# Kernel tuning notes

Measured on AMD Instinct MI355X. Metric: run time of the kernel, lower is better.

## Reference

```python
import jax, jax.numpy as jnp
import numpy as np

B, CAP, D, A, K = 512, 50000, 256, 18, 5
LAM = 0.5  # ration_lambda


def setup_inputs() -> dict:
    key = jax.random.key(0)
    ks = jax.random.split(key, 14)
    def w(k, shape, fan_in):
        return jax.random.normal(k, shape, dtype=jnp.float32) / np.sqrt(fan_in)
    inp = {
        'x': jax.random.normal(ks[0], (B, 4, 84, 84), dtype=jnp.float32),
        'conv1_w': w(ks[1], (32, 4, 8, 8), 4 * 8 * 8),
        'conv1_b': jnp.zeros((32,), jnp.float32),
        'conv2_w': w(ks[2], (64, 32, 4, 4), 32 * 4 * 4),
        'conv2_b': jnp.zeros((64,), jnp.float32),
        'conv3_w': w(ks[3], (64, 64, 3, 3), 64 * 3 * 3),
        'conv3_b': jnp.zeros((64,), jnp.float32),
        'fc_w': w(ks[4], (3136, D), 3136),
        'fc_b': jnp.zeros((D,), jnp.float32),
        'out_w': w(ks[5], (D, A), D),
        'out_b': jnp.zeros((A,), jnp.float32),
        # value buffer: stored embeddings (post-ReLU, nonnegative) and Q values
        'buf_emb': jax.random.uniform(ks[6], (CAP, D), dtype=jnp.float32),
        'buf_q': jax.random.normal(ks[7], (CAP, A), dtype=jnp.float32),
    }
    return inp


def _conv_relu(x, w, b, stride):
    y = jax.lax.conv_general_dilated(
        x, w, window_strides=(stride, stride), padding='VALID',
        dimension_numbers=('NCHW', 'OIHW', 'NCHW'))
    return jax.nn.relu(y + b[None, :, None, None])


def reference(x, conv1_w, conv1_b, conv2_w, conv2_b, conv3_w, conv3_b,
              fc_w, fc_b, out_w, out_b, buf_emb, buf_q):
    # LargeAtariCNN: 84->20->9->7 spatial, ReLU everywhere incl. final linear
    h = _conv_relu(x, conv1_w, conv1_b, 4)   # [B,32,20,20]
    h = _conv_relu(h, conv2_w, conv2_b, 2)   # [B,64,9,9]
    h = _conv_relu(h, conv3_w, conv3_b, 1)   # [B,64,7,7]
    h = h.reshape(h.shape[0], -1)            # [B,3136]
    h = jax.nn.relu(h @ fc_w + fc_b)         # [B,D] embedding
    q = h @ out_w + out_b                    # [B,A] parametric Q
    # kNN over value buffer: squared L2 distances [B,CAP]
    d2 = (jnp.sum(h * h, axis=1, keepdims=True)
          - 2.0 * (h @ buf_emb.T)
          + jnp.sum(buf_emb * buf_emb, axis=1)[None, :])
    _, idx = jax.lax.top_k(-d2, K)           # K nearest, [B,K]
    non_param_q = jnp.mean(buf_q[idx], axis=1)  # [B,K,A] -> [B,A]
    q_blend = LAM * q + (1.0 - LAM) * non_param_q
    return (q_blend, h)
```

## Files before the change

### kernel.cpp

```cpp
#include <hip/hip_runtime.h>
#include <hip/hip_bf16.h>

#define FINF 3.402823466e38f

typedef short bf16x8 __attribute__((ext_vector_type(8)));
typedef float f32x4 __attribute__((ext_vector_type(4)));

__device__ __forceinline__ unsigned short f2bf_rne(float f) {
  unsigned u = __float_as_uint(f);
  unsigned r = u + 0x7fff + ((u >> 16) & 1);
  return (unsigned short)(r >> 16);
}
__device__ __forceinline__ float bf2f(unsigned short u) {
  return __uint_as_float(((unsigned)u) << 16);
}
__device__ __forceinline__ unsigned long long shflx64(unsigned long long v, int m) {
  unsigned lo = __shfl_xor((unsigned)(v & 0xFFFFFFFFu), m, 64);
  unsigned hi = __shfl_xor((unsigned)(v >> 32), m, 64);
  return (((unsigned long long)hi) << 32) | lo;
}
__device__ __forceinline__ void lds_barrier() {
  asm volatile("s_waitcnt lgkmcnt(0)" ::: "memory");
  __builtin_amdgcn_s_barrier();
  __builtin_amdgcn_sched_barrier(0);
}
__device__ __forceinline__ void wave_sync() {
  asm volatile("s_waitcnt lgkmcnt(0)" ::: "memory");
  __builtin_amdgcn_sched_barrier(0);
}
__device__ __forceinline__ void gload16(const unsigned short* g, short* l) {
  __builtin_amdgcn_global_load_lds(
      (const __attribute__((address_space(1))) unsigned int*)g,
      (__attribute__((address_space(3))) unsigned int*)l, 16, 0, 0);
}

__global__ __launch_bounds__(128) void w1swz_k(const float* __restrict__ w1,
                                               unsigned short* __restrict__ bh,
                                               unsigned short* __restrict__ bl) {
  int ky = blockIdx.x;
  int t = threadIdx.x, nf = t >> 6, l = t & 63;
  int oc = nf * 16 + (l & 15), ic = l >> 4;
  bf16x8 hv, lv;
#pragma unroll
  for (int j = 0; j < 8; ++j) {
    float v = w1[((oc * 4 + ic) * 8 + ky) * 8 + j];
    unsigned short h = f2bf_rne(v);
    hv[j] = (short)h;
    lv[j] = (short)f2bf_rne(v - bf2f(h));
  }
  *(bf16x8*)(&bh[((size_t)(ky * 2 + nf) * 64 + l) * 8]) = hv;
  *(bf16x8*)(&bl[((size_t)(ky * 2 + nf) * 64 + l) * 8]) = lv;
}

__global__ __launch_bounds__(256) void conv1m_k(
    const float* __restrict__ x,
    const unsigned short* __restrict__ bh, const unsigned short* __restrict__ bl,
    const float* __restrict__ bias, unsigned short* __restrict__ h1s) {
  __shared__ short As[256 * 72];
  int t = threadIdx.x, w = t >> 6, lane = t & 63, lm = lane & 15, hi4 = lane >> 4;
  int m = blockIdx.x * 256 + t;
  int n = m / 400, p = m % 400, oy = p / 20, ox = p % 20;
  size_t xoff = (size_t)n * 28224 + (size_t)(oy * 4) * 84 + ox * 4;
  f32x4 acc[4][2];
#pragma unroll
  for (int mf = 0; mf < 4; ++mf)
#pragma unroll
    for (int nf = 0; nf < 2; ++nf) acc[mf][nf] = (f32x4){0.f, 0.f, 0.f, 0.f};

  float4 fa[8];
#pragma unroll
  for (int ic = 0; ic < 4; ++ic) {
    fa[ic * 2 + 0] = *(const float4*)(x + xoff + ic * 7056);
    fa[ic * 2 + 1] = *(const float4*)(x + xoff + ic * 7056 + 4);
  }
  const unsigned short* bfp = bh + (size_t)lane * 8;
  const unsigned short* blp = bl + (size_t)lane * 8;
  bf16x8 cbh[2], cbl[2];
#pragma unroll
  for (int nf = 0; nf < 2; ++nf) {
    cbh[nf] = *(const bf16x8*)(bfp + nf * 512);
    cbl[nf] = *(const bf16x8*)(blp + nf * 512);
  }
#pragma unroll
  for (int ky = 0; ky < 8; ++ky) {
    if (ky) wave_sync();
    {
      short* wp = &As[t * 72];
#pragma unroll
      for (int ic = 0; ic < 4; ++ic) {
        float e0 = fa[ic * 2].x, e1 = fa[ic * 2].y, e2 = fa[ic * 2].z, e3 = fa[ic * 2].w;
        float e4 = fa[ic * 2 + 1].x, e5 = fa[ic * 2 + 1].y, e6 = fa[ic * 2 + 1].z, e7 = fa[ic * 2 + 1].w;
        bf16x8 hv, lv;
        unsigned short h;
        h = f2bf_rne(e0); hv[0] = (short)h; lv[0] = (short)f2bf_rne(e0 - bf2f(h));
        h = f2bf_rne(e1); hv[1] = (short)h; lv[1] = (short)f2bf_rne(e1 - bf2f(h));
        h = f2bf_rne(e2); hv[2] = (short)h; lv[2] = (short)f2bf_rne(e2 - bf2f(h));
        h = f2bf_rne(e3); hv[3] = (short)h; lv[3] = (short)f2bf_rne(e3 - bf2f(h));
        h = f2bf_rne(e4); hv[4] = (short)h; lv[4] = (short)f2bf_rne(e4 - bf2f(h));
        h = f2bf_rne(e5); hv[5] = (short)h; lv[5] = (short)f2bf_rne(e5 - bf2f(h));
        h = f2bf_rne(e6); hv[6] = (short)h; lv[6] = (short)f2bf_rne(e6 - bf2f(h));
        h = f2bf_rne(e7); hv[7] = (short)h; lv[7] = (short)f2bf_rne(e7 - bf2f(h));
        *(bf16x8*)(wp + ic * 8) = hv;
        *(bf16x8*)(wp + 36 + ic * 8) = lv;
      }
    }
    wave_sync();
    bf16x8 nbh[2], nbl[2];
    if (ky < 7) {
      size_t ap = xoff + (size_t)(ky + 1) * 84;
#pragma unroll
      for (int ic = 0; ic < 4; ++ic) {
        fa[ic * 2 + 0] = *(const float4*)(x + ap + ic * 7056);
        fa[ic * 2 + 1] = *(const float4*)(x + ap + ic * 7056 + 4);
      }
#pragma unroll
      for (int nf = 0; nf < 2; ++nf) {
        nbh[nf] = *(const bf16x8*)(bfp + ((ky + 1) * 2 + nf) * 512);
        nbl[nf] = *(const bf16x8*)(blp + ((ky + 1) * 2 + nf) * 512);
      }
    }
    bf16x8 ah[4], al[4];
#pragma unroll
    for (int mf = 0; mf < 4; ++mf) {
      const short* rp = &As[(w * 64 + mf * 16 + lm) * 72 + hi4 * 8];
      ah[mf] = *(const bf16x8*)(rp);
      al[mf] = *(const bf16x8*)(rp + 36);
    }
#pragma unroll
    for (int mf = 0; mf < 4; ++mf)
#pragma unroll
      for (int nf = 0; nf < 2; ++nf) {
        acc[mf][nf] = __builtin_amdgcn_mfma_f32_16x16x32_bf16(ah[mf], cbh[nf], acc[mf][nf], 0, 0, 0);
        acc[mf][nf] = __builtin_amdgcn_mfma_f32_16x16x32_bf16(ah[mf], cbl[nf], acc[mf][nf], 0, 0, 0);
        acc[mf][nf] = __builtin_amdgcn_mfma_f32_16x16x32_bf16(al[mf], cbh[nf], acc[mf][nf], 0, 0, 0);
      }
    if (ky < 7) {
#pragma unroll
      for (int nf = 0; nf < 2; ++nf) { cbh[nf] = nbh[nf]; cbl[nf] = nbl[nf]; }
    }
  }
  float bv[2];
#pragma unroll
  for (int nf = 0; nf < 2; ++nf) bv[nf] = bias[nf * 16 + lm];
#pragma unroll
  for (int mf = 0; mf < 4; ++mf)
#pragma unroll
    for (int nf = 0; nf < 2; ++nf)
#pragma unroll
      for (int r = 0; r < 4; ++r) {
        size_t mrow = (size_t)blockIdx.x * 256 + w * 64 + mf * 16 + hi4 * 4 + r;
        float v = fmaxf(acc[mf][nf][r] + bv[nf], 0.f);
        unsigned short h = f2bf_rne(v);
        h1s[mrow * 64 + nf * 16 + lm] = h;
        h1s[mrow * 64 + 32 + nf * 16 + lm] = f2bf_rne(v - bf2f(h));
      }
}

__global__ __launch_bounds__(256) void w2swz_k(const float* __restrict__ w2,
                                               unsigned short* __restrict__ bh,
                                               unsigned short* __restrict__ bl) {
  int tap = blockIdx.x, ky = tap >> 2, kx = tap & 3;
  int t = threadIdx.x, nf = t >> 6, l = t & 63;
  int oc = nf * 16 + (l & 15);
  bf16x8 hv, lv;
#pragma unroll
  for (int j = 0; j < 8; ++j) {
    int ic = (l >> 4) * 8 + j;
    float v = w2[((oc * 32 + ic) * 4 + ky) * 4 + kx];
    unsigned short h = f2bf_rne(v);
    hv[j] = (short)h;
    lv[j] = (short)f2bf_rne(v - bf2f(h));
  }
  *(bf16x8*)(&bh[((size_t)(tap * 4 + nf) * 64 + l) * 8]) = hv;
  *(bf16x8*)(&bl[((size_t)(tap * 4 + nf) * 64 + l) * 8]) = lv;
}

__global__ __launch_bounds__(256) void w3swz_k(const float* __restrict__ w3,
                                               unsigned short* __restrict__ bh,
                                               unsigned short* __restrict__ bl) {
  int tt = blockIdx.x, tap = tt >> 1, half = tt & 1, ky = tap / 3, kx = tap % 3;
  int t = threadIdx.x, nf = t >> 6, l = t & 63;
  int oc = nf * 16 + (l & 15);
  bf16x8 hv, lv;
#pragma unroll
  for (int j = 0; j < 8; ++j) {
    int ic = half * 32 + (l >> 4) * 8 + j;
    float v = w3[((oc * 64 + ic) * 3 + ky) * 3 + kx];
    unsigned short h = f2bf_rne(v);
    hv[j] = (short)h;
    lv[j] = (short)f2bf_rne(v - bf2f(h));
  }
  *(bf16x8*)(&bh[((size_t)(tt * 4 + nf) * 64 + l) * 8]) = hv;
  *(bf16x8*)(&bl[((size_t)(tt * 4 + nf) * 64 + l) * 8]) = lv;
}

__global__ __launch_bounds__(256) void conv2m_k(
    const unsigned short* __restrict__ h1s, const unsigned short* __restrict__ bh,
    const unsigned short* __restrict__ bl, const float* __restrict__ bias,
    unsigned short* __restrict__ h2s) {
  __shared__ short As[256 * 72];
  int t = threadIdx.x, w = t >> 6, lane = t & 63, lm = lane & 15, hi4 = lane >> 4;
  int m = blockIdx.x * 256 + t;
  int n = m / 81, p = m % 81, oy = p / 9, ox = p % 9;
  const unsigned short* abase = h1s + (size_t)(n * 400 + oy * 40 + ox * 2) * 64;
  f32x4 acc[4][4];
#pragma unroll
  for (int mf = 0; mf < 4; ++mf)
#pragma unroll
    for (int nf = 0; nf < 4; ++nf) acc[mf][nf] = (f32x4){0.f, 0.f, 0.f, 0.f};

  bf16x8 s0, s1, s2, s3, s4, s5, s6, s7;
  {
    const unsigned short* ap = abase;
    s0 = *(const bf16x8*)(ap);      s1 = *(const bf16x8*)(ap + 8);
    s2 = *(const bf16x8*)(ap + 16); s3 = *(const bf16x8*)(ap + 24);
    s4 = *(const bf16x8*)(ap + 32); s5 = *(const bf16x8*)(ap + 40);
    s6 = *(const bf16x8*)(ap + 48); s7 = *(const bf16x8*)(ap + 56);
  }
  const unsigned short* bfp = bh + (size_t)lane * 8;
  const unsigned short* blp = bl + (size_t)lane * 8;
  bf16x8 cbh[4], cbl[4];
#pragma unroll
  for (int nf = 0; nf < 4; ++nf) {
    cbh[nf] = *(const bf16x8*)(bfp + nf * 512);
    cbl[nf] = *(const bf16x8*)(blp + nf * 512);
  }
#pragma unroll
  for (int tap = 0; tap < 16; ++tap) {
    if (tap) wave_sync();
    {
      short* wp = &As[t * 72];
      *(bf16x8*)(wp) = s0;      *(bf16x8*)(wp + 8) = s1;
      *(bf16x8*)(wp + 16) = s2; *(bf16x8*)(wp + 24) = s3;
      *(bf16x8*)(wp + 36) = s4; *(bf16x8*)(wp + 44) = s5;
      *(bf16x8*)(wp + 52) = s6; *(bf16x8*)(wp + 60) = s7;
    }
    wave_sync();
    bf16x8 nbh[4], nbl[4];
    if (tap < 15) {
      const unsigned short* ap = abase + (((tap + 1) >> 2) * 1280 + ((tap + 1) & 3) * 64);
      s0 = *(const bf16x8*)(ap);      s1 = *(const bf16x8*)(ap + 8);
      s2 = *(const bf16x8*)(ap + 16); s3 = *(const bf16x8*)(ap + 24);
      s4 = *(const bf16x8*)(ap + 32); s5 = *(const bf16x8*)(ap + 40);
      s6 = *(const bf16x8*)(ap + 48); s7 = *(const bf16x8*)(ap + 56);
#pragma unroll
      for (int nf = 0; nf < 4; ++nf) {
        nbh[nf] = *(const bf16x8*)(bfp + ((tap + 1) * 4 + nf) * 512);
        nbl[nf] = *(const bf16x8*)(blp + ((tap + 1) * 4 + nf) * 512);
      }
    }
    bf16x8 ah[4], al[4];
#pragma unroll
    for (int mf = 0; mf < 4; ++mf) {
      const short* rp = &As[(w * 64 + mf * 16 + lm) * 72 + hi4 * 8];
      ah[mf] = *(const bf16x8*)(rp);
      al[mf] = *(const bf16x8*)(rp + 36);
    }
#pragma unroll
    for (int mf = 0; mf < 4; ++mf)
#pragma unroll
      for (int nf = 0; nf < 4; ++nf) {
        acc[mf][nf] = __builtin_amdgcn_mfma_f32_16x16x32_bf16(ah[mf], cbh[nf], acc[mf][nf], 0, 0, 0);
        acc[mf][nf] = __builtin_amdgcn_mfma_f32_16x16x32_bf16(ah[mf], cbl[nf], acc[mf][nf], 0, 0, 0);
        acc[mf][nf] = __builtin_amdgcn_mfma_f32_16x16x32_bf16(al[mf], cbh[nf], acc[mf][nf], 0, 0, 0);
      }
    if (tap < 15) {
#pragma unroll
      for (int nf = 0; nf < 4; ++nf) { cbh[nf] = nbh[nf]; cbl[nf] = nbl[nf]; }
    }
  }
  float bv[4];
#pragma unroll
  for (int nf = 0; nf < 4; ++nf) bv[nf] = bias[nf * 16 + lm];
#pragma unroll
  for (int mf = 0; mf < 4; ++mf)
#pragma unroll
    for (int nf = 0; nf < 4; ++nf)
#pragma unroll
      for (int r = 0; r < 4; ++r) {
        size_t mrow = (size_t)blockIdx.x * 256 + w * 64 + mf * 16 + hi4 * 4 + r;
        float v = fmaxf(acc[mf][nf][r] + bv[nf], 0.f);
        unsigned short h = f2bf_rne(v);
        h2s[mrow * 128 + nf * 16 + lm] = h;
        h2s[mrow * 128 + 64 + nf * 16 + lm] = f2bf_rne(v - bf2f(h));
      }
}

__global__ __launch_bounds__(256) void conv3m_k(
    const unsigned short* __restrict__ h2s, const unsigned short* __restrict__ bh,
    const unsigned short* __restrict__ bl, const float* __restrict__ bias,
    unsigned short* __restrict__ h3hi, unsigned short* __restrict__ h3lo) {
  __shared__ short As[256 * 72];
  int t = threadIdx.x, w = t >> 6, lane = t & 63, lm = lane & 15, hi4 = lane >> 4;
  int m = blockIdx.x * 256 + t;
  int n = m / 49, p = m % 49, oy = p / 7, ox = p % 7;
  const unsigned short* abase = h2s + (size_t)(n * 81 + oy * 9 + ox) * 128;
  f32x4 acc[4][4];
#pragma unroll
  for (int mf = 0; mf < 4; ++mf)
#pragma unroll
    for (int nf = 0; nf < 4; ++nf) acc[mf][nf] = (f32x4){0.f, 0.f, 0.f, 0.f};

  bf16x8 s0, s1, s2, s3, s4, s5, s6, s7;
  {
    const unsigned short* ap = abase;
    s0 = *(const bf16x8*)(ap);      s1 = *(const bf16x8*)(ap + 8);
    s2 = *(const bf16x8*)(ap + 16); s3 = *(const bf16x8*)(ap + 24);
    s4 = *(const bf16x8*)(ap + 64); s5 = *(const bf16x8*)(ap + 72);
    s6 = *(const bf16x8*)(ap + 80); s7 = *(const bf16x8*)(ap + 88);
  }
  const unsigned short* bfp = bh + (size_t)lane * 8;
  const unsigned short* blp = bl + (size_t)lane * 8;
  bf16x8 cbh[4], cbl[4];
#pragma unroll
  for (int nf = 0; nf < 4; ++nf) {
    cbh[nf] = *(const bf16x8*)(bfp + nf * 512);
    cbl[nf] = *(const bf16x8*)(blp + nf * 512);
  }
#pragma unroll
  for (int tt = 0; tt < 18; ++tt) {
    if (tt) wave_sync();
    {
      short* wp = &As[t * 72];
      *(bf16x8*)(wp) = s0;      *(bf16x8*)(wp + 8) = s1;
      *(bf16x8*)(wp + 16) = s2; *(bf16x8*)(wp + 24) = s3;
      *(bf16x8*)(wp + 36) = s4; *(bf16x8*)(wp + 44) = s5;
      *(bf16x8*)(wp + 52) = s6; *(bf16x8*)(wp + 60) = s7;
    }
    wave_sync();
    bf16x8 nbh[4], nbl[4];
    if (tt < 17) {
      const int tn = tt + 1, tapn = tn >> 1, halfn = tn & 1;
      const unsigned short* ap = abase + ((tapn / 3) * 9 + (tapn % 3)) * 128 + halfn * 32;
      s0 = *(const bf16x8*)(ap);      s1 = *(const bf16x8*)(ap + 8);
      s2 = *(const bf16x8*)(ap + 16); s3 = *(const bf16x8*)(ap + 24);
      s4 = *(const bf16x8*)(ap + 64); s5 = *(const bf16x8*)(ap + 72);
      s6 = *(const bf16x8*)(ap + 80); s7 = *(const bf16x8*)(ap + 88);
#pragma unroll
      for (int nf = 0; nf < 4; ++nf) {
        nbh[nf] = *(const bf16x8*)(bfp + ((tt + 1) * 4 + nf) * 512);
        nbl[nf] = *(const bf16x8*)(blp + ((tt + 1) * 4 + nf) * 512);
      }
    }
    bf16x8 ah[4], al[4];
#pragma unroll
    for (int mf = 0; mf < 4; ++mf) {
      const short* rp = &As[(w * 64 + mf * 16 + lm) * 72 + hi4 * 8];
      ah[mf] = *(const bf16x8*)(rp);
      al[mf] = *(const bf16x8*)(rp + 36);
    }
#pragma unroll
    for (int mf = 0; mf < 4; ++mf)
#pragma unroll
      for (int nf = 0; nf < 4; ++nf) {
        acc[mf][nf] = __builtin_amdgcn_mfma_f32_16x16x32_bf16(ah[mf], cbh[nf], acc[mf][nf], 0, 0, 0);
        acc[mf][nf] = __builtin_amdgcn_mfma_f32_16x16x32_bf16(ah[mf], cbl[nf], acc[mf][nf], 0, 0, 0);
        acc[mf][nf] = __builtin_amdgcn_mfma_f32_16x16x32_bf16(al[mf], cbh[nf], acc[mf][nf], 0, 0, 0);
      }
    if (tt < 17) {
#pragma unroll
      for (int nf = 0; nf < 4; ++nf) { cbh[nf] = nbh[nf]; cbl[nf] = nbl[nf]; }
    }
  }
  float bv[4];
#pragma unroll
  for (int nf = 0; nf < 4; ++nf) bv[nf] = bias[nf * 16 + lm];
#pragma unroll
  for (int mf = 0; mf < 4; ++mf)
#pragma unroll
    for (int nf = 0; nf < 4; ++nf)
#pragma unroll
      for (int r = 0; r < 4; ++r) {
        size_t mrow = (size_t)blockIdx.x * 256 + w * 64 + mf * 16 + hi4 * 4 + r;
        float v = fmaxf(acc[mf][nf][r] + bv[nf], 0.f);
        unsigned short h = f2bf_rne(v);
        h3hi[mrow * 64 + nf * 16 + lm] = h;
        h3lo[mrow * 64 + nf * 16 + lm] = f2bf_rne(v - bf2f(h));
      }
}

__global__ __launch_bounds__(256) void fcwcvt_k(const float* __restrict__ fw,
                                                unsigned short* __restrict__ fwhi,
                                                unsigned short* __restrict__ fwlo) {
  __shared__ float tile[64][65];
  int p = blockIdx.x, nb = blockIdx.y;
  int t = threadIdx.x;
#pragma unroll
  for (int i = 0; i < 16; ++i) {
    int c = (t >> 6) * 16 + i;
    tile[c][t & 63] = fw[(c * 49 + p) * 256 + nb * 64 + (t & 63)];
  }
  __syncthreads();
#pragma unroll
  for (int i = 0; i < 16; ++i) {
    int n2 = (t >> 6) * 16 + i, c2 = t & 63;
    float v = tile[c2][n2];
    unsigned short h = f2bf_rne(v);
    size_t o = (size_t)(nb * 64 + n2) * 3136 + p * 64 + c2;
    fwhi[o] = h;
    fwlo[o] = f2bf_rne(v - bf2f(h));
  }
}

__global__ __launch_bounds__(256) void fc2_k(
    const unsigned short* __restrict__ h3hi, const unsigned short* __restrict__ h3lo,
    const unsigned short* __restrict__ fwhi, const unsigned short* __restrict__ fwlo,
    float* __restrict__ hpre) {
  int t = threadIdx.x, w = t >> 6, lane = t & 63, lm = lane & 15, hi4 = lane >> 4;
  int b = blockIdx.x, mb = b / 14, kc = b % 14;
  int m0 = mb * 64, n0 = w * 64;
  size_t kof = (size_t)kc * 224 + hi4 * 8;
  const unsigned short* pah[4]; const unsigned short* pal[4];
  const unsigned short* pbh[4]; const unsigned short* pbl[4];
#pragma unroll
  for (int mf = 0; mf < 4; ++mf) {
    pah[mf] = h3hi + (size_t)(m0 + mf * 16 + lm) * 3136 + kof;
    pal[mf] = h3lo + (size_t)(m0 + mf * 16 + lm) * 3136 + kof;
  }
#pragma unroll
  for (int nf = 0; nf < 4; ++nf) {
    pbh[nf] = fwhi + (size_t)(n0 + nf * 16 + lm) * 3136 + kof;
    pbl[nf] = fwlo + (size_t)(n0 + nf * 16 + lm) * 3136 + kof;
  }
  f32x4 acc[4][4];
#pragma unroll
  for (int mf = 0; mf < 4; ++mf)
#pragma unroll
    for (int nf = 0; nf < 4; ++nf) acc[mf][nf] = (f32x4){0.f, 0.f, 0.f, 0.f};
  bf16x8 cah[4], cal[4], cbh[4], cbl[4];
#pragma unroll
  for (int i = 0; i < 4; ++i) {
    cah[i] = *(const bf16x8*)(pah[i]); cal[i] = *(const bf16x8*)(pal[i]);
    cbh[i] = *(const bf16x8*)(pbh[i]); cbl[i] = *(const bf16x8*)(pbl[i]);
  }
#pragma unroll
  for (int ks = 0; ks < 7; ++ks) {
    bf16x8 nah[4], nal[4], nbh[4], nbl[4];
    if (ks < 6) {
      const int off = (ks + 1) * 32;
#pragma unroll
      for (int i = 0; i < 4; ++i) {
        nah[i] = *(const bf16x8*)(pah[i] + off); nal[i] = *(const bf16x8*)(pal[i] + off);
        nbh[i] = *(const bf16x8*)(pbh[i] + off); nbl[i] = *(const bf16x8*)(pbl[i] + off);
      }
    }
#pragma unroll
    for (int mf = 0; mf < 4; ++mf)
#pragma unroll
      for (int nf = 0; nf < 4; ++nf) {
        acc[mf][nf] = __builtin_amdgcn_mfma_f32_16x16x32_bf16(cah[mf], cbh[nf], acc[mf][nf], 0, 0, 0);
        acc[mf][nf] = __builtin_amdgcn_mfma_f32_16x16x32_bf16(cah[mf], cbl[nf], acc[mf][nf], 0, 0, 0);
        acc[mf][nf] = __builtin_amdgcn_mfma_f32_16x16x32_bf16(cal[mf], cbh[nf], acc[mf][nf], 0, 0, 0);
      }
    if (ks < 6) {
#pragma unroll
      for (int i = 0; i < 4; ++i) {
        cah[i] = nah[i]; cal[i] = nal[i]; cbh[i] = nbh[i]; cbl[i] = nbl[i];
      }
    }
  }
  float* outp = hpre + (size_t)kc * 131072;
#pragma unroll
  for (int mf = 0; mf < 4; ++mf)
#pragma unroll
    for (int nf = 0; nf < 4; ++nf)
#pragma unroll
      for (int r = 0; r < 4; ++r)
        outp[(m0 + mf * 16 + hi4 * 4 + r) * 256 + n0 + nf * 16 + lm] = acc[mf][nf][r];
}

__global__ __launch_bounds__(256) void fc_post_k(
    const float* __restrict__ hpre, const float* __restrict__ fb,
    float* __restrict__ hout, unsigned short* __restrict__ a_split) {
  int m = blockIdx.x, n = threadIdx.x;
  float v = fb[n];
#pragma unroll
  for (int kc = 0; kc < 14; ++kc) v += hpre[(size_t)kc * 131072 + m * 256 + n];
  v = fmaxf(v, 0.f);
  hout[m * 256 + n] = v;
  unsigned short hi = f2bf_rne(v);
  unsigned short lo = f2bf_rne(v - bf2f(hi));
  a_split[(size_t)m * 768 + n] = hi;
  a_split[(size_t)m * 768 + 256 + n] = hi;
  a_split[(size_t)m * 768 + 512 + n] = lo;
}

__global__ __launch_bounds__(256) void embcvt_k(const float* __restrict__ e,
                                                unsigned short* __restrict__ Bemb,
                                                float* __restrict__ nrm) {
  int row = blockIdx.x * 4 + (threadIdx.x >> 6);
  if (row >= 50000) return;
  int lane = threadIdx.x & 63;
  float4 v = ((const float4*)(e + row * 256))[lane];
  float s = v.x * v.x + v.y * v.y + v.z * v.z + v.w * v.w;
  unsigned short h0 = f2bf_rne(v.x), h1 = f2bf_rne(v.y), h2 = f2bf_rne(v.z), h3 = f2bf_rne(v.w);
  unsigned short l0 = f2bf_rne(v.x - bf2f(h0)), l1 = f2bf_rne(v.y - bf2f(h1));
  unsigned short l2 = f2bf_rne(v.z - bf2f(h2)), l3 = f2bf_rne(v.w - bf2f(h3));
  *(ushort4*)(Bemb + (size_t)row * 512 + lane * 4) = make_ushort4(h0, h1, h2, h3);
  *(ushort4*)(Bemb + (size_t)row * 512 + 256 + lane * 4) = make_ushort4(l0, l1, l2, l3);
  for (int off = 32; off > 0; off >>= 1) s += __shfl_down(s, off);
  if (lane == 0) nrm[row] = s;
}

__global__ __launch_bounds__(256) void dist3_k(
    const unsigned short* __restrict__ a_split, const unsigned short* __restrict__ Bemb,
    const float* __restrict__ nrm, unsigned long long* __restrict__ cand) {
  __shared__ short Ah[8192];
  __shared__ short Al[8192];
  __shared__ short Bh[8192];
  __shared__ short Bl[8192];
  int t = threadIdx.x, w = t >> 6, lane = t & 63, lm = lane & 15, hi = lane >> 4;
  int mw = w >> 1, nw = w & 1;
  int b = blockIdx.x;
  int p = (b & 7) * 196 + (b >> 3);
  int nb = p >> 2, mb = p & 3;

  const unsigned short* aTile = a_split + (size_t)mb * 128 * 768;
  const unsigned short* bTile = Bemb + (size_t)nb * 128 * 512;

  int crow[4], csl[4];
#pragma unroll
  for (int i = 0; i < 4; ++i) {
    int p16 = (w * 4 + i) * 64 + lane;
    crow[i] = p16 >> 3;
    csl[i] = ((p16 & 7) ^ (crow[i] & 7)) * 8;
  }

  f32x4 acc[4][4];
#pragma unroll
  for (int nf = 0; nf < 4; ++nf)
#pragma unroll
    for (int mf = 0; mf < 4; ++mf) acc[nf][mf] = (f32x4){0.f, 0.f, 0.f, 0.f};

  const int arow0 = mw * 64;
  const int brow0 = nw * 64;

#pragma unroll
  for (int i = 0; i < 4; ++i) {
    gload16(aTile + (size_t)crow[i] * 768 + csl[i], &Ah[(w * 4 + i) * 512]);
    gload16(aTile + (size_t)crow[i] * 768 + 512 + csl[i], &Al[(w * 4 + i) * 512]);
    gload16(bTile + (size_t)crow[i] * 512 + csl[i], &Bh[(w * 4 + i) * 512]);
    gload16(bTile + (size_t)crow[i] * 512 + 256 + csl[i], &Bl[(w * 4 + i) * 512]);
  }

#pragma unroll
  for (int kk = 0; kk < 4; ++kk) {
    asm volatile("s_waitcnt vmcnt(0)" ::: "memory");
    __builtin_amdgcn_s_barrier();
    __builtin_amdgcn_sched_barrier(0);
#pragma unroll
    for (int q2 = 0; q2 < 2; ++q2) {
      bf16x8 fah[4], fal[4], fbh[4], fbl[4];
#pragma unroll
      for (int mf = 0; mf < 4; ++mf) {
        int row = arow0 + mf * 16 + lm;
        int off = row * 64 + (((q2 * 4 + hi) ^ (lm & 7)) * 8);
        fah[mf] = *(const bf16x8*)(&Ah[off]);
        fal[mf] = *(const bf16x8*)(&Al[off]);
      }
#pragma unroll
      for (int nf = 0; nf < 4; ++nf) {
        int row = brow0 + nf * 16 + lm;
        int off = row * 64 + (((q2 * 4 + hi) ^ (lm & 7)) * 8);
        fbh[nf] = *(const bf16x8*)(&Bh[off]);
        fbl[nf] = *(const bf16x8*)(&Bl[off]);
      }
#pragma unroll
      for (int nf = 0; nf < 4; ++nf)
#pragma unroll
        for (int mf = 0; mf < 4; ++mf) {
          acc[nf][mf] = __builtin_amdgcn_mfma_f32_16x16x32_bf16(fbh[nf], fah[mf], acc[nf][mf], 0, 0, 0);
          acc[nf][mf] = __builtin_amdgcn_mfma_f32_16x16x32_bf16(fbl[nf], fah[mf], acc[nf][mf], 0, 0, 0);
          acc[nf][mf] = __builtin_amdgcn_mfma_f32_16x16x32_bf16(fbh[nf], fal[mf], acc[nf][mf], 0, 0, 0);
        }
    }
    if (kk < 3) {
      lds_barrier();
      const int ko = (kk + 1) * 64;
#pragma unroll
      for (int i = 0; i < 4; ++i) {
        gload16(aTile + (size_t)crow[i] * 768 + ko + csl[i], &Ah[(w * 4 + i) * 512]);
        gload16(aTile + (size_t)crow[i] * 768 + 512 + ko + csl[i], &Al[(w * 4 + i) * 512]);
        gload16(bTile + (size_t)crow[i] * 512 + ko + csl[i], &Bh[(w * 4 + i) * 512]);
        gload16(bTile + (size_t)crow[i] * 512 + 256 + ko + csl[i], &Bl[(w * 4 + i) * 512]);
      }
    }
  }

  const int nbase = nb * 128 + nw * 64;
  const int mbase = mb * 128 + mw * 64;
  unsigned long long Lst[4][5];
#pragma unroll
  for (int mf = 0; mf < 4; ++mf)
#pragma unroll
    for (int j = 0; j < 5; ++j) Lst[mf][j] = ~0ull;

#pragma unroll
  for (int nf = 0; nf < 4; ++nf) {
    int n0 = nbase + nf * 16 + hi * 4;
    float4 nv = *(const float4*)(nrm + n0);
#pragma unroll
    for (int r = 0; r < 4; ++r) {
      int n = n0 + r;
      bool ok = n < 50000;
      float nvr = (r == 0) ? nv.x : (r == 1) ? nv.y : (r == 2) ? nv.z : nv.w;
#pragma unroll
      for (int mf = 0; mf < 4; ++mf) {
        float sc = nvr - 2.f * acc[nf][mf][r];
        unsigned u = __float_as_uint(sc);
        u = ((int)u < 0) ? ~u : (u | 0x80000000u);
        unsigned long long k = ok ? ((((unsigned long long)u) << 32) | (unsigned)n) : ~0ull;
        if (k < Lst[mf][4]) {
          bool b3 = k < Lst[mf][3], b2 = k < Lst[mf][2], b1 = k < Lst[mf][1], b0 = k < Lst[mf][0];
          Lst[mf][4] = b3 ? Lst[mf][3] : k;
          Lst[mf][3] = b3 ? (b2 ? Lst[mf][2] : k) : Lst[mf][3];
          Lst[mf][2] = b2 ? (b1 ? Lst[mf][1] : k) : Lst[mf][2];
          Lst[mf][1] = b1 ? (b0 ? Lst[mf][0] : k) : Lst[mf][1];
          Lst[mf][0] = b0 ? k : Lst[mf][0];
        }
      }
    }
  }
#pragma unroll
  for (int mf = 0; mf < 4; ++mf) {
#pragma unroll
    for (int s = 16; s <= 32; s <<= 1) {
      unsigned long long b0 = shflx64(Lst[mf][0], s), b1 = shflx64(Lst[mf][1], s),
                         b2 = shflx64(Lst[mf][2], s), b3 = shflx64(Lst[mf][3], s),
                         b4 = shflx64(Lst[mf][4], s);
      unsigned long long a0 = Lst[mf][0], a1 = Lst[mf][1], a2 = Lst[mf][2],
                         a3 = Lst[mf][3], a4 = Lst[mf][4];
#pragma unroll
      for (int j = 0; j < 5; ++j) {
        bool ta = a0 <= b0;
        Lst[mf][j] = ta ? a0 : b0;
        unsigned long long na0 = ta ? a1 : a0, na1 = ta ? a2 : a1, na2 = ta ? a3 : a2, na3 = ta ? a4 : a3;
        unsigned long long nb0 = ta ? b0 : b1, nb1 = ta ? b1 : b2, nb2 = ta ? b2 : b3, nb3 = ta ? b3 : b4;
        a0 = na0; a1 = na1; a2 = na2; a3 = na3;
        b0 = nb0; b1 = nb1; b2 = nb2; b3 = nb3;
      }
    }
  }
  if (lane < 16) {
#pragma unroll
    for (int mf = 0; mf < 4; ++mf) {
      size_t base = ((size_t)(mbase + mf * 16 + lm) * 784 + (nb * 2 + nw)) * 5;
#pragma unroll
      for (int j = 0; j < 5; ++j) cand[base + j] = Lst[mf][j];
    }
  }
}

__global__ __launch_bounds__(64) void merge2_k(
    const unsigned long long* __restrict__ cand, const float* __restrict__ hbuf,
    const float* __restrict__ bufq, const float* __restrict__ out_w,
    const float* __restrict__ out_b, float* __restrict__ qout) {
  int row = blockIdx.x, lane = threadIdx.x;
  unsigned long long L0 = ~0ull, L1 = ~0ull, L2 = ~0ull, L3 = ~0ull, L4 = ~0ull;
  const unsigned long long* cr = cand + (size_t)row * 3920;
  for (int i = lane; i < 3920; i += 64) {
    unsigned long long k = cr[i];
    if (k < L4) {
      bool b3 = k < L3, b2 = k < L2, b1 = k < L1, b0 = k < L0;
      L4 = b3 ? L3 : k;
      L3 = b3 ? (b2 ? L2 : k) : L3;
      L2 = b2 ? (b1 ? L1 : k) : L2;
      L1 = b1 ? (b0 ? L0 : k) : L1;
      L0 = b0 ? k : L0;
    }
  }
#pragma unroll
  for (int s = 1; s < 64; s <<= 1) {
    unsigned long long o0 = shflx64(L0, s), o1 = shflx64(L1, s), o2 = shflx64(L2, s),
                       o3 = shflx64(L3, s), o4 = shflx64(L4, s);
    unsigned long long a0 = L0, a1 = L1, a2 = L2, a3 = L3, a4 = L4;
    unsigned long long b0 = o0, b1 = o1, b2 = o2, b3 = o3, b4 = o4;
    unsigned long long m[5];
#pragma unroll
    for (int j = 0; j < 5; ++j) {
      bool ta = a0 <= b0;
      m[j] = ta ? a0 : b0;
      unsigned long long na0 = ta ? a1 : a0, na1 = ta ? a2 : a1, na2 = ta ? a3 : a2, na3 = ta ? a4 : a3;
      unsigned long long nb0 = ta ? b0 : b1, nb1 = ta ? b1 : b2, nb2 = ta ? b2 : b3, nb3 = ta ? b3 : b4;
      a0 = na0; a1 = na1; a2 = na2; a3 = na3;
      b0 = nb0; b1 = nb1; b2 = nb2; b3 = nb3;
    }
    L0 = m[0]; L1 = m[1]; L2 = m[2]; L3 = m[3]; L4 = m[4];
  }
  int i0 = (int)(L0 & 0xFFFFFFFFu), i1 = (int)(L1 & 0xFFFFFFFFu), i2 = (int)(L2 & 0xFFFFFFFFu);
  int i3 = (int)(L3 & 0xFFFFFFFFu), i4 = (int)(L4 & 0xFFFFFFFFu);
  if (lane < 18) {
    float np = 0.2f * (bufq[(size_t)i0 * 18 + lane] + bufq[(size_t)i1 * 18 + lane] +
                       bufq[(size_t)i2 * 18 + lane] + bufq[(size_t)i3 * 18 + lane] +
                       bufq[(size_t)i4 * 18 + lane]);
    const float* hr = hbuf + row * 256;
    float q = out_b[lane];
    for (int d = 0; d < 256; ++d) q += hr[d] * out_w[d * 18 + lane];
    qout[row * 18 + lane] = 0.5f * q + 0.5f * np;
  }
}

__global__ __launch_bounds__(320) void conv1_k(
    const float* __restrict__ x, const float* __restrict__ w,
    const float* __restrict__ b, float* __restrict__ y) {
  __shared__ float x_s[4 * 84 * 84];
  int n = blockIdx.x;
  {
    const float4* src = (const float4*)(x + n * 28224);
    float4* dst = (float4*)x_s;
    for (int i = threadIdx.x; i < 7056; i += 320) dst[i] = src[i];
  }
  __syncthreads();
  int t = threadIdx.x;
  int ocg = t / 80, rem = t % 80, oy = rem / 4, oxg = rem % 4;
  float acc[8][5];
#pragma unroll
  for (int r = 0; r < 8; ++r) {
    float bv = b[ocg * 8 + r];
#pragma unroll
    for (int i = 0; i < 5; ++i) acc[r][i] = bv;
  }
  for (int ic = 0; ic < 4; ++ic) {
    for (int ky = 0; ky < 8; ++ky) {
      const float* xrow = x_s + ic * 7056 + (oy * 4 + ky) * 84 + oxg * 20;
      const float* wrow = w + ic * 64 + ky * 8;
#pragma unroll
      for (int kx = 0; kx < 8; ++kx) {
        float xv[5];
#pragma unroll
        for (int i = 0; i < 5; ++i) xv[i] = xrow[i * 4 + kx];
#pragma unroll
        for (int r = 0; r < 8; ++r) {
          float wv = wrow[(ocg * 8 + r) * 256 + kx];
#pragma unroll
          for (int i = 0; i < 5; ++i) acc[r][i] += wv * xv[i];
        }
      }
    }
  }
  float* yb = y + n * 12800 + oy * 20 + oxg * 5;
#pragma unroll
  for (int r = 0; r < 8; ++r)
#pragma unroll
    for (int i = 0; i < 5; ++i)
      yb[(ocg * 8 + r) * 400 + i] = fmaxf(acc[r][i], 0.f);
}

__global__ __launch_bounds__(256) void conv2_k(
    const float* __restrict__ h1, const float* __restrict__ w,
    const float* __restrict__ b, float* __restrict__ y) {
  __shared__ float x_s[32 * 400];
  int n = blockIdx.x;
  {
    const float4* src = (const float4*)(h1 + n * 12800);
    float4* dst = (float4*)x_s;
    for (int i = threadIdx.x; i < 3200; i += 256) dst[i] = src[i];
  }
  __syncthreads();
  int t = threadIdx.x;
  if (t < 216) {
    int ocg = t / 27, rem = t % 27, oy = rem / 3, oxg = rem % 3;
    float acc[8][3];
#pragma unroll
    for (int r = 0; r < 8; ++r) {
      float bv = b[ocg * 8 + r];
#pragma unroll
      for (int i = 0; i < 3; ++i) acc[r][i] = bv;
    }
    const float* xbase = x_s + (oy * 2) * 20 + oxg * 6;
    for (int ic = 0; ic < 32; ++ic) {
#pragma unroll
      for (int ky = 0; ky < 4; ++ky) {
        const float* xr = xbase + ic * 400 + ky * 20;
        const float* wr = w + ic * 16 + ky * 4;
#pragma unroll
        for (int kx = 0; kx < 4; ++kx) {
          float xv0 = xr[kx], xv1 = xr[kx + 2], xv2 = xr[kx + 4];
#pragma unroll
          for (int r = 0; r < 8; ++r) {
            float wv = wr[(ocg * 8 + r) * 512 + kx];
            acc[r][0] += wv * xv0;
            acc[r][1] += wv * xv1;
            acc[r][2] += wv * xv2;
          }
        }
      }
    }
    float* yb = y + n * 5184 + oy * 9 + oxg * 3;
#pragma unroll
    for (int r = 0; r < 8; ++r)
#pragma unroll
      for (int i = 0; i < 3; ++i)
        yb[(ocg * 8 + r) * 81 + i] = fmaxf(acc[r][i], 0.f);
  }
}

__global__ __launch_bounds__(128) void conv3_k(
    const float* __restrict__ h2, const float* __restrict__ w,
    const float* __restrict__ b, float* __restrict__ y) {
  __shared__ float x_s[64 * 81];
  int n = blockIdx.x;
  {
    const float4* src = (const float4*)(h2 + n * 5184);
    float4* dst = (float4*)x_s;
    for (int i = threadIdx.x; i < 1296; i += 128) dst[i] = src[i];
  }
  __syncthreads();
  int t = threadIdx.x;
  if (t < 112) {
    int ocg = t / 7, oy = t % 7;
    float acc[4][7];
#pragma unroll
    for (int r = 0; r < 4; ++r) {
      float bv = b[ocg * 4 + r];
#pragma unroll
      for (int i = 0; i < 7; ++i) acc[r][i] = bv;
    }
    for (int ic = 0; ic < 64; ++ic) {
#pragma unroll
      for (int ky = 0; ky < 3; ++ky) {
        const float* xr = x_s + ic * 81 + (oy + ky) * 9;
        float xv[9];
#pragma unroll
        for (int i = 0; i < 9; ++i) xv[i] = xr[i];
        const float* wr = w + ic * 9 + ky * 3;
#pragma unroll
        for (int kx = 0; kx < 3; ++kx) {
#pragma unroll
          for (int r = 0; r < 4; ++r) {
            float wv = wr[(ocg * 4 + r) * 576 + kx];
#pragma unroll
            for (int i = 0; i < 7; ++i) acc[r][i] += wv * xv[i + kx];
          }
        }
      }
    }
    float* yb = y + n * 3136 + oy * 7;
#pragma unroll
    for (int r = 0; r < 4; ++r)
#pragma unroll
      for (int i = 0; i < 7; ++i)
        yb[(ocg * 4 + r) * 49 + i] = fmaxf(acc[r][i], 0.f);
  }
}

__global__ __launch_bounds__(256) void fc_k(
    const float* __restrict__ h3, const float* __restrict__ fw,
    const float* __restrict__ fb, float* __restrict__ hout,
    unsigned short* __restrict__ a_split) {
  __shared__ float a_s[4 * 3136];
  int n0 = blockIdx.x * 4;
  {
    const float4* src = (const float4*)(h3 + n0 * 3136);
    float4* dst = (float4*)a_s;
    for (int i = threadIdx.x; i < 3136; i += 256) dst[i] = src[i];
  }
  __syncthreads();
  int j = threadIdx.x;
  float a0 = fb[j], a1 = a0, a2 = a0, a3 = a0;
  for (int k = 0; k < 3136; ++k) {
    float wv = fw[k * 256 + j];
    a0 += a_s[k] * wv;
    a1 += a_s[3136 + k] * wv;
    a2 += a_s[2 * 3136 + k] * wv;
    a3 += a_s[3 * 3136 + k] * wv;
  }
  float hv[4];
  hv[0] = fmaxf(a0, 0.f); hv[1] = fmaxf(a1, 0.f);
  hv[2] = fmaxf(a2, 0.f); hv[3] = fmaxf(a3, 0.f);
#pragma unroll
  for (int r = 0; r < 4; ++r) {
    hout[(n0 + r) * 256 + j] = hv[r];
    if (a_split) {
      unsigned short hi = f2bf_rne(hv[r]);
      unsigned short lo = f2bf_rne(hv[r] - bf2f(hi));
      a_split[(size_t)(n0 + r) * 768 + j] = hi;
      a_split[(size_t)(n0 + r) * 768 + 256 + j] = hi;
      a_split[(size_t)(n0 + r) * 768 + 512 + j] = lo;
    }
  }
}

__global__ __launch_bounds__(256) void norm_k(const float* __restrict__ e,
                                              float* __restrict__ nrm) {
  int row = blockIdx.x * 4 + (threadIdx.x >> 6);
  if (row >= 50000) return;
  int lane = threadIdx.x & 63;
  float4 v = ((const float4*)(e + row * 256))[lane];
  float s = v.x * v.x + v.y * v.y + v.z * v.z + v.w * v.w;
  for (int off = 32; off > 0; off >>= 1) s += __shfl_down(s, off);
  if (lane == 0) nrm[row] = s;
}

__global__ __launch_bounds__(256) void dist_topk_k(
    const float* __restrict__ hbuf, const float* __restrict__ emb,
    const float* __restrict__ nrm, float* __restrict__ cand_d,
    int* __restrict__ cand_i) {
  __shared__ float a_s[16 * 256];
  __shared__ float b_s[512 * 17];
  int rb = blockIdx.x & 31, cb = blockIdx.x >> 5;
  int t = threadIdx.x;
  {
    const float4* src = (const float4*)(hbuf + rb * 16 * 256);
    float4* dst = (float4*)a_s;
    for (int i = t; i < 1024; i += 256) dst[i] = src[i];
  }
  float acc[8][4];
#pragma unroll
  for (int r = 0; r < 8; ++r)
#pragma unroll
    for (int c = 0; c < 4; ++c) acc[r][c] = 0.f;
  int ct = t & 127, rt = t >> 7;
  for (int kb = 0; kb < 256; kb += 16) {
    __syncthreads();
    for (int i = t; i < 2048; i += 256) {
      int j = i >> 2, kq = i & 3;
      int jg = cb * 512 + j;
      float4 v = make_float4(0.f, 0.f, 0.f, 0.f);
      if (jg < 50000) v = *(const float4*)(emb + jg * 256 + kb + kq * 4);
      float* dst = b_s + j * 17 + kq * 4;
      dst[0] = v.x; dst[1] = v.y; dst[2] = v.z; dst[3] = v.w;
    }
    __syncthreads();
#pragma unroll
    for (int k = 0; k < 16; ++k) {
      float av[8];
#pragma unroll
      for (int r = 0; r < 8; ++r) av[r] = a_s[(rt * 8 + r) * 256 + kb + k];
#pragma unroll
      for (int cc = 0; cc < 4; ++cc) {
        float bv = b_s[(ct + cc * 128) * 17 + k];
#pragma unroll
        for (int r = 0; r < 8; ++r) acc[r][cc] += av[r] * bv;
      }
    }
  }
  __syncthreads();
  float* score = b_s;
#pragma unroll
  for (int cc = 0; cc < 4; ++cc) {
    int c = ct + cc * 128;
    int jg = cb * 512 + c;
    float nv = (jg < 50000) ? nrm[jg] : 0.f;
#pragma unroll
    for (int r = 0; r < 8; ++r)
      score[(rt * 8 + r) * 512 + c] = (jg < 50000) ? (nv - 2.f * acc[r][cc]) : FINF;
  }
  __syncthreads();
  int wave = t >> 6, lane = t & 63;
  for (int rr = 0; rr < 4; ++rr) {
    int r = wave * 4 + rr;
    float v[8];
#pragma unroll
    for (int i = 0; i < 8; ++i) v[i] = score[r * 512 + lane + i * 64];
    for (int it = 0; it < 5; ++it) {
      float bv = v[0];
      int bc = lane;
#pragma unroll
      for (int i = 1; i < 8; ++i) {
        float xv = v[i];
        int c = lane + i * 64;
        if (xv < bv) { bv = xv; bc = c; }
      }
      for (int off = 32; off > 0; off >>= 1) {
        float ov = __shfl_down(bv, off);
        int ocx = __shfl_down(bc, off);
        if (ov < bv || (ov == bv && ocx < bc)) { bv = ov; bc = ocx; }
      }
      bv = __shfl(bv, 0);
      bc = __shfl(bc, 0);
      if (lane == 0) {
        int row_g = rb * 16 + r;
        int slot = (row_g * 98 + cb) * 5 + it;
        cand_d[slot] = bv;
        cand_i[slot] = cb * 512 + bc;
      }
#pragma unroll
      for (int i = 0; i < 8; ++i)
        if (lane + i * 64 == bc) v[i] = FINF;
    }
  }
}

__global__ __launch_bounds__(64) void merge_k(
    const float* __restrict__ cand_d, const int* __restrict__ cand_i,
    const float* __restrict__ hbuf, const float* __restrict__ bufq,
    const float* __restrict__ out_w, const float* __restrict__ out_b,
    float* __restrict__ qout) {
  int row = blockIdx.x, lane = threadIdx.x;
  __shared__ float sd[490];
  __shared__ int si[490];
  __shared__ int win[5];
  for (int i = lane; i < 490; i += 64) {
    sd[i] = cand_d[row * 490 + i];
    si[i] = cand_i[row * 490 + i];
  }
  __syncthreads();
  float v[8];
  int ix[8];
#pragma unroll
  for (int i = 0; i < 8; ++i) {
    int s = lane + i * 64;
    v[i] = (s < 490) ? sd[s] : FINF;
    ix[i] = (s < 490) ? si[s] : 0x7fffffff;
  }
  for (int it = 0; it < 5; ++it) {
    float bv = v[0];
    int bi = ix[0];
#pragma unroll
    for (int i = 1; i < 8; ++i)
      if (v[i] < bv || (v[i] == bv && ix[i] < bi)) { bv = v[i]; bi = ix[i]; }
    for (int off = 32; off > 0; off >>= 1) {
      float ov = __shfl_down(bv, off);
      int oi = __shfl_down(bi, off);
      if (ov < bv || (ov == bv && oi < bi)) { bv = ov; bi = oi; }
    }
    bi = __shfl(bi, 0);
    if (lane == 0) win[it] = bi;
#pragma unroll
    for (int i = 0; i < 8; ++i)
      if (ix[i] == bi) v[i] = FINF;
  }
  __syncthreads();
  if (lane < 18) {
    float np = 0.f;
#pragma unroll
    for (int it = 0; it < 5; ++it) np += bufq[win[it] * 18 + lane];
    np *= 0.2f;
    const float* hr = hbuf + row * 256;
    float q = out_b[lane];
    for (int d = 0; d < 256; ++d) q += hr[d] * out_w[d * 18 + lane];
    qout[row * 18 + lane] = 0.5f * q + 0.5f * np;
  }
}

extern "C" void kernel_launch(void* const* d_in, const int* in_sizes, int n_in,
                              void* d_out, int out_size, void* d_ws, size_t ws_size,
                              hipStream_t stream) {
  const float* x       = (const float*)d_in[0];
  const float* conv1_w = (const float*)d_in[1];
  const float* conv1_b = (const float*)d_in[2];
  const float* conv2_w = (const float*)d_in[3];
  const float* conv2_b = (const float*)d_in[4];
  const float* conv3_w = (const float*)d_in[5];
  const float* conv3_b = (const float*)d_in[6];
  const float* fc_w    = (const float*)d_in[7];
  const float* fc_b    = (const float*)d_in[8];
  const float* out_w   = (const float*)d_in[9];
  const float* out_b   = (const float*)d_in[10];
  const float* buf_emb = (const float*)d_in[11];
  const float* buf_q   = (const float*)d_in[12];

  float* out = (float*)d_out;
  float* hout = out + 9216;

  float* ws = (float*)d_ws;
  unsigned short* h1s  = (unsigned short*)(ws);
  unsigned short* h2s  = (unsigned short*)(ws + 6553600);
  unsigned short* h3hi = (unsigned short*)(ws);
  unsigned short* h3lo = (unsigned short*)(ws + 802816);
  unsigned short* Bs1h = (unsigned short*)(ws + 6553600);
  unsigned short* Bs1l = (unsigned short*)(ws + 6557696);
  float* nrm = ws + 9207808;
  unsigned long long* cand = (unsigned long long*)(ws + 9257984);
  unsigned short* Bs2h = (unsigned short*)(ws + 9257984);
  unsigned short* Bs2l = (unsigned short*)(ws + 9274368);
  unsigned short* Bs3h = (unsigned short*)(ws + 9290752);
  unsigned short* Bs3l = (unsigned short*)(ws + 9309184);
  unsigned short* fwhi = (unsigned short*)(ws + 9327616);
  unsigned short* fwlo = (unsigned short*)(ws + 9729024);
  float* hpre = ws + 10130432;
  unsigned short* a_split = (unsigned short*)(ws + 13272064);
  unsigned short* Bemb = (unsigned short*)(ws + 13468672);
  const size_t NEED = 105254912ull;

  bool mfma_path = (ws_size >= NEED);

  if (mfma_path) {
    w1swz_k<<<8, 128, 0, stream>>>(conv1_w, Bs1h, Bs1l);
    w2swz_k<<<16, 256, 0, stream>>>(conv2_w, Bs2h, Bs2l);
    w3swz_k<<<18, 256, 0, stream>>>(conv3_w, Bs3h, Bs3l);
    fcwcvt_k<<<dim3(49, 4), 256, 0, stream>>>(fc_w, fwhi, fwlo);
    embcvt_k<<<12500, 256, 0, stream>>>(buf_emb, Bemb, nrm);
    conv1m_k<<<800, 256, 0, stream>>>(x, Bs1h, Bs1l, conv1_b, h1s);
    conv2m_k<<<162, 256, 0, stream>>>(h1s, Bs2h, Bs2l, conv2_b, h2s);
    conv3m_k<<<98, 256, 0, stream>>>(h2s, Bs3h, Bs3l, conv3_b, h3hi, h3lo);
    fc2_k<<<112, 256, 0, stream>>>(h3hi, h3lo, fwhi, fwlo, hpre);
    fc_post_k<<<512, 256, 0, stream>>>(hpre, fc_b, hout, a_split);
    dist3_k<<<1568, 256, 0, stream>>>(a_split, Bemb, nrm, cand);
    merge2_k<<<512, 64, 0, stream>>>(cand, hout, buf_q, out_w, out_b, out);
  } else {
    float* h1 = ws;
    float* h2 = h1 + 6553600;
    float* h3 = ws;
    float* nrm_o = h2 + 2654208;
    float* cand_d = nrm_o + 50000;
    int* cand_i = (int*)(cand_d + 250880);
    conv1_k<<<512, 320, 0, stream>>>(x, conv1_w, conv1_b, h1);
    conv2_k<<<512, 256, 0, stream>>>(h1, conv2_w, conv2_b, h2);
    conv3_k<<<512, 128, 0, stream>>>(h2, conv3_w, conv3_b, h3);
    fc_k<<<128, 256, 0, stream>>>(h3, fc_w, fc_b, hout, nullptr);
    norm_k<<<12500, 256, 0, stream>>>(buf_emb, nrm_o);
    dist_topk_k<<<3136, 256, 0, stream>>>(hout, buf_emb, nrm_o, cand_d, cand_i);
    merge_k<<<512, 64, 0, stream>>>(cand_d, cand_i, hout, buf_q, out_w, out_b, out);
  }
}
```

Measured before the change: 251.3 us.

## Merge weight-prep kernels, compact a_split layout, raise MFMA priority in dist3

Combines the four weight swizzle/convert kernels into one prep_k launch, which removes three kernel launches and their gaps. The a_split buffer drops its duplicated hi copy, going from a 768 to a 512 row stride, which cuts the bytes written by fc_post and read by dist3. It also wraps dist3's MFMA block in s_setprio(1)/s_setprio(0) so waves doing math get scheduling priority over waves issuing loads. The prep kernel has branch-divergent blocks, and block 0-7 idles half its threads.

```diff
diff --git a/kernel.cpp b/kernel.cpp
--- a/kernel.cpp
+++ b/kernel.cpp
@@ -34,22 +34,77 @@
       (__attribute__((address_space(3))) unsigned int*)l, 16, 0, 0);
 }
 
-__global__ __launch_bounds__(128) void w1swz_k(const float* __restrict__ w1,
-                                               unsigned short* __restrict__ bh,
-                                               unsigned short* __restrict__ bl) {
-  int ky = blockIdx.x;
-  int t = threadIdx.x, nf = t >> 6, l = t & 63;
-  int oc = nf * 16 + (l & 15), ic = l >> 4;
-  bf16x8 hv, lv;
-#pragma unroll
-  for (int j = 0; j < 8; ++j) {
-    float v = w1[((oc * 4 + ic) * 8 + ky) * 8 + j];
-    unsigned short h = f2bf_rne(v);
-    hv[j] = (short)h;
-    lv[j] = (short)f2bf_rne(v - bf2f(h));
-  }
-  *(bf16x8*)(&bh[((size_t)(ky * 2 + nf) * 64 + l) * 8]) = hv;
-  *(bf16x8*)(&bl[((size_t)(ky * 2 + nf) * 64 + l) * 8]) = lv;
+__global__ __launch_bounds__(256) void prep_k(
+    const float* __restrict__ w1, unsigned short* __restrict__ b1h, unsigned short* __restrict__ b1l,
+    const float* __restrict__ w2, unsigned short* __restrict__ b2h, unsigned short* __restrict__ b2l,
+    const float* __restrict__ w3, unsigned short* __restrict__ b3h, unsigned short* __restrict__ b3l,
+    const float* __restrict__ fw, unsigned short* __restrict__ fwhi, unsigned short* __restrict__ fwlo) {
+  __shared__ float tile[64][65];
+  int b = blockIdx.x, t = threadIdx.x;
+  if (b < 8) {
+    if (t < 128) {
+      int ky = b;
+      int nf = t >> 6, l = t & 63;
+      int oc = nf * 16 + (l & 15), ic = l >> 4;
+      bf16x8 hv, lv;
+#pragma unroll
+      for (int j = 0; j < 8; ++j) {
+        float v = w1[((oc * 4 + ic) * 8 + ky) * 8 + j];
+        unsigned short h = f2bf_rne(v);
+        hv[j] = (short)h;
+        lv[j] = (short)f2bf_rne(v - bf2f(h));
+      }
+      *(bf16x8*)(&b1h[((size_t)(ky * 2 + nf) * 64 + l) * 8]) = hv;
+      *(bf16x8*)(&b1l[((size_t)(ky * 2 + nf) * 64 + l) * 8]) = lv;
+    }
+  } else if (b < 24) {
+    int tap = b - 8, ky = tap >> 2, kx = tap & 3;
+    int nf = t >> 6, l = t & 63;
+    int oc = nf * 16 + (l & 15);
+    bf16x8 hv, lv;
+#pragma unroll
+    for (int j = 0; j < 8; ++j) {
+      int ic = (l >> 4) * 8 + j;
+      float v = w2[((oc * 32 + ic) * 4 + ky) * 4 + kx];
+      unsigned short h = f2bf_rne(v);
+      hv[j] = (short)h;
+      lv[j] = (short)f2bf_rne(v - bf2f(h));
+    }
+    *(bf16x8*)(&b2h[((size_t)(tap * 4 + nf) * 64 + l) * 8]) = hv;
+    *(bf16x8*)(&b2l[((size_t)(tap * 4 + nf) * 64 + l) * 8]) = lv;
+  } else if (b < 42) {
+    int tt = b - 24, tap = tt >> 1, half = tt & 1, ky = tap / 3, kx = tap % 3;
+    int nf = t >> 6, l = t & 63;
+    int oc = nf * 16 + (l & 15);
+    bf16x8 hv, lv;
+#pragma unroll
+    for (int j = 0; j < 8; ++j) {
+      int ic = half * 32 + (l >> 4) * 8 + j;
+      float v = w3[((oc * 64 + ic) * 3 + ky) * 3 + kx];
+      unsigned short h = f2bf_rne(v);
+      hv[j] = (short)h;
+      lv[j] = (short)f2bf_rne(v - bf2f(h));
+    }
+    *(bf16x8*)(&b3h[((size_t)(tt * 4 + nf) * 64 + l) * 8]) = hv;
+    *(bf16x8*)(&b3l[((size_t)(tt * 4 + nf) * 64 + l) * 8]) = lv;
+  } else {
+    int idx = b - 42, p = idx % 49, nb = idx / 49;
+#pragma unroll
+    for (int i = 0; i < 16; ++i) {
+      int c = (t >> 6) * 16 + i;
+      tile[c][t & 63] = fw[(c * 49 + p) * 256 + nb * 64 + (t & 63)];
+    }
+    __syncthreads();
+#pragma unroll
+    for (int i = 0; i < 16; ++i) {
+      int n2 = (t >> 6) * 16 + i, c2 = t & 63;
+      float v = tile[c2][n2];
+      unsigned short h = f2bf_rne(v);
+      size_t o = (size_t)(nb * 64 + n2) * 3136 + p * 64 + c2;
+      fwhi[o] = h;
+      fwlo[o] = f2bf_rne(v - bf2f(h));
+    }
+  }
 }
 
 __global__ __launch_bounds__(256) void conv1m_k(
@@ -156,44 +211,6 @@
       }
 }
 
-__global__ __launch_bounds__(256) void w2swz_k(const float* __restrict__ w2,
-                                               unsigned short* __restrict__ bh,
-                                               unsigned short* __restrict__ bl) {
-  int tap = blockIdx.x, ky = tap >> 2, kx = tap & 3;
-  int t = threadIdx.x, nf = t >> 6, l = t & 63;
-  int oc = nf * 16 + (l & 15);
-  bf16x8 hv, lv;
-#pragma unroll
-  for (int j = 0; j < 8; ++j) {
-    int ic = (l >> 4) * 8 + j;
-    float v = w2[((oc * 32 + ic) * 4 + ky) * 4 + kx];
-    unsigned short h = f2bf_rne(v);
-    hv[j] = (short)h;
-    lv[j] = (short)f2bf_rne(v - bf2f(h));
-  }
-  *(bf16x8*)(&bh[((size_t)(tap * 4 + nf) * 64 + l) * 8]) = hv;
-  *(bf16x8*)(&bl[((size_t)(tap * 4 + nf) * 64 + l) * 8]) = lv;
-}
-
-__global__ __launch_bounds__(256) void w3swz_k(const float* __restrict__ w3,
-                                               unsigned short* __restrict__ bh,
-                                               unsigned short* __restrict__ bl) {
-  int tt = blockIdx.x, tap = tt >> 1, half = tt & 1, ky = tap / 3, kx = tap % 3;
-  int t = threadIdx.x, nf = t >> 6, l = t & 63;
-  int oc = nf * 16 + (l & 15);
-  bf16x8 hv, lv;
-#pragma unroll
-  for (int j = 0; j < 8; ++j) {
-    int ic = half * 32 + (l >> 4) * 8 + j;
-    float v = w3[((oc * 64 + ic) * 3 + ky) * 3 + kx];
-    unsigned short h = f2bf_rne(v);
-    hv[j] = (short)h;
-    lv[j] = (short)f2bf_rne(v - bf2f(h));
-  }
-  *(bf16x8*)(&bh[((size_t)(tt * 4 + nf) * 64 + l) * 8]) = hv;
-  *(bf16x8*)(&bl[((size_t)(tt * 4 + nf) * 64 + l) * 8]) = lv;
-}
-
 __global__ __launch_bounds__(256) void conv2m_k(
     const unsigned short* __restrict__ h1s, const unsigned short* __restrict__ bh,
     const unsigned short* __restrict__ bl, const float* __restrict__ bias,
@@ -379,29 +396,6 @@
       }
 }
 
-__global__ __launch_bounds__(256) void fcwcvt_k(const float* __restrict__ fw,
-                                                unsigned short* __restrict__ fwhi,
-                                                unsigned short* __restrict__ fwlo) {
-  __shared__ float tile[64][65];
-  int p = blockIdx.x, nb = blockIdx.y;
-  int t = threadIdx.x;
-#pragma unroll
-  for (int i = 0; i < 16; ++i) {
-    int c = (t >> 6) * 16 + i;
-    tile[c][t & 63] = fw[(c * 49 + p) * 256 + nb * 64 + (t & 63)];
-  }
-  __syncthreads();
-#pragma unroll
-  for (int i = 0; i < 16; ++i) {
-    int n2 = (t >> 6) * 16 + i, c2 = t & 63;
-    float v = tile[c2][n2];
-    unsigned short h = f2bf_rne(v);
-    size_t o = (size_t)(nb * 64 + n2) * 3136 + p * 64 + c2;
-    fwhi[o] = h;
-    fwlo[o] = f2bf_rne(v - bf2f(h));
-  }
-}
-
 __global__ __launch_bounds__(256) void fc2_k(
     const unsigned short* __restrict__ h3hi, const unsigned short* __restrict__ h3lo,
     const unsigned short* __restrict__ fwhi, const unsigned short* __restrict__ fwlo,
@@ -480,9 +474,8 @@
   hout[m * 256 + n] = v;
   unsigned short hi = f2bf_rne(v);
   unsigned short lo = f2bf_rne(v - bf2f(hi));
-  a_split[(size_t)m * 768 + n] = hi;
-  a_split[(size_t)m * 768 + 256 + n] = hi;
-  a_split[(size_t)m * 768 + 512 + n] = lo;
+  a_split[(size_t)m * 512 + n] = hi;
+  a_split[(size_t)m * 512 + 256 + n] = lo;
 }
 
 __global__ __launch_bounds__(256) void embcvt_k(const float* __restrict__ e,
@@ -515,7 +508,7 @@
   int p = (b & 7) * 196 + (b >> 3);
   int nb = p >> 2, mb = p & 3;
 
-  const unsigned short* aTile = a_split + (size_t)mb * 128 * 768;
+  const unsigned short* aTile = a_split + (size_t)mb * 128 * 512;
   const unsigned short* bTile = Bemb + (size_t)nb * 128 * 512;
 
   int crow[4], csl[4];
@@ -537,8 +530,8 @@
 
 #pragma unroll
   for (int i = 0; i < 4; ++i) {
-    gload16(aTile + (size_t)crow[i] * 768 + csl[i], &Ah[(w * 4 + i) * 512]);
-    gload16(aTile + (size_t)crow[i] * 768 + 512 + csl[i], &Al[(w * 4 + i) * 512]);
+    gload16(aTile + (size_t)crow[i] * 512 + csl[i], &Ah[(w * 4 + i) * 512]);
+    gload16(aTile + (size_t)crow[i] * 512 + 256 + csl[i], &Al[(w * 4 + i) * 512]);
     gload16(bTile + (size_t)crow[i] * 512 + csl[i], &Bh[(w * 4 + i) * 512]);
     gload16(bTile + (size_t)crow[i] * 512 + 256 + csl[i], &Bl[(w * 4 + i) * 512]);
   }
@@ -565,6 +558,7 @@
         fbh[nf] = *(const bf16x8*)(&Bh[off]);
         fbl[nf] = *(const bf16x8*)(&Bl[off]);
       }
+      __builtin_amdgcn_s_setprio(1);
 #pragma unroll
       for (int nf = 0; nf < 4; ++nf)
 #pragma unroll
@@ -573,14 +567,15 @@
           acc[nf][mf] = __builtin_amdgcn_mfma_f32_16x16x32_bf16(fbl[nf], fah[mf], acc[nf][mf], 0, 0, 0);
           acc[nf][mf] = __builtin_amdgcn_mfma_f32_16x16x32_bf16(fbh[nf], fal[mf], acc[nf][mf], 0, 0, 0);
         }
+      __builtin_amdgcn_s_setprio(0);
     }
     if (kk < 3) {
       lds_barrier();
       const int ko = (kk + 1) * 64;
 #pragma unroll
       for (int i = 0; i < 4; ++i) {
-        gload16(aTile + (size_t)crow[i] * 768 + ko + csl[i], &Ah[(w * 4 + i) * 512]);
-        gload16(aTile + (size_t)crow[i] * 768 + 512 + ko + csl[i], &Al[(w * 4 + i) * 512]);
+        gload16(aTile + (size_t)crow[i] * 512 + ko + csl[i], &Ah[(w * 4 + i) * 512]);
+        gload16(aTile + (size_t)crow[i] * 512 + 256 + ko + csl[i], &Al[(w * 4 + i) * 512]);
         gload16(bTile + (size_t)crow[i] * 512 + ko + csl[i], &Bh[(w * 4 + i) * 512]);
         gload16(bTile + (size_t)crow[i] * 512 + 256 + ko + csl[i], &Bl[(w * 4 + i) * 512]);
       }
@@ -874,9 +869,8 @@
     if (a_split) {
       unsigned short hi = f2bf_rne(hv[r]);
       unsigned short lo = f2bf_rne(hv[r] - bf2f(hi));
-      a_split[(size_t)(n0 + r) * 768 + j] = hi;
-      a_split[(size_t)(n0 + r) * 768 + 256 + j] = hi;
-      a_split[(size_t)(n0 + r) * 768 + 512 + j] = lo;
+      a_split[(size_t)(n0 + r) * 512 + j] = hi;
+      a_split[(size_t)(n0 + r) * 512 + 256 + j] = lo;
     }
   }
 }
@@ -1077,10 +1071,8 @@
   bool mfma_path = (ws_size >= NEED);
 
   if (mfma_path) {
-    w1swz_k<<<8, 128, 0, stream>>>(conv1_w, Bs1h, Bs1l);
-    w2swz_k<<<16, 256, 0, stream>>>(conv2_w, Bs2h, Bs2l);
-    w3swz_k<<<18, 256, 0, stream>>>(conv3_w, Bs3h, Bs3l);
-    fcwcvt_k<<<dim3(49, 4), 256, 0, stream>>>(fc_w, fwhi, fwlo);
+    prep_k<<<238, 256, 0, stream>>>(conv1_w, Bs1h, Bs1l, conv2_w, Bs2h, Bs2l,
+                                    conv3_w, Bs3h, Bs3l, fc_w, fwhi, fwlo);
     embcvt_k<<<12500, 256, 0, stream>>>(buf_emb, Bemb, nrm);
     conv1m_k<<<800, 256, 0, stream>>>(x, Bs1h, Bs1l, conv1_b, h1s);
     conv2m_k<<<162, 256, 0, stream>>>(h1s, Bs2h, Bs2l, conv2_b, h2s);
```

Measured after the change: 241.8 us. -3.8%, faster.
